# Kernel optimization log

Measured on AMD Instinct MI355X. Metric: run time of the kernel, lower is better.

The kernel has to match this reference:

```python
import jax, jax.numpy as jnp
import numpy as np

N_NODES = 16384


def gcn_conv(x, edge_index, W, b):
    """GCNConv: out = D^{-1/2} (A + I) D^{-1/2} (x @ W) + b."""
    n = x.shape[0]
    xw = x @ W  # [n, out_dim] -- transform before propagate (PyG order)
    loops = jnp.arange(n)
    src = jnp.concatenate([edge_index[0], loops])
    dst = jnp.concatenate([edge_index[1], loops])
    ones = jnp.ones(src.shape[0], dtype=xw.dtype)
    deg = jax.ops.segment_sum(ones, dst, num_segments=n)  # degree incl. self-loops
    dinv = jnp.where(deg > 0, jax.lax.rsqrt(deg), 0.0)
    norm = dinv[src] * dinv[dst]  # [E + n]
    msg = xw[src] * norm[:, None]  # gather + scale
    out = jax.ops.segment_sum(msg, dst, num_segments=n)  # scatter-add aggregate
    return out + b


def setup_inputs() -> dict:
    key = jax.random.key(0)
    ks = jax.random.split(key, 8)
    N, E, C = N_NODES, 524288, 7
    x = jax.random.normal(ks[0], (N, N), dtype=jnp.float32)
    edge_index = jax.random.randint(ks[1], (2, E), 0, N, dtype=jnp.int64)
    W1 = jax.random.normal(ks[2], (N, 50), dtype=jnp.float32) * (1.0 / np.sqrt(N))
    b1 = jnp.zeros((50,), dtype=jnp.float32)
    W2 = jax.random.normal(ks[3], (50, 2), dtype=jnp.float32) * (1.0 / np.sqrt(50))
    b2 = jnp.zeros((2,), dtype=jnp.float32)
    Wc = jax.random.normal(ks[4], (2, C), dtype=jnp.float32) * (1.0 / np.sqrt(2))
    bc = jnp.zeros((C,), dtype=jnp.float32)
    return {"x": x, "edge_index": edge_index, "W1": W1, "b1": b1,
            "W2": W2, "b2": b2, "Wc": Wc, "bc": bc}


def reference(x, edge_index, W1, b1, W2, b2, Wc, bc):
    h = jnp.tanh(gcn_conv(x, edge_index, W1, b1))   # [N, 50]
    h = jnp.tanh(gcn_conv(h, edge_index, W2, b2))   # [N, 2]
    out = h @ Wc + bc                               # [N, num_classes]
    return (out, h)
```

## Files before the change

kernel.cpp:

```cpp
#include <hip/hip_runtime.h>

typedef float  f32x4  __attribute__((ext_vector_type(4)));
typedef __bf16 bf16x8 __attribute__((ext_vector_type(8)));

#define N_NODES 16384
#define K_DIM   16384
#define H1_DIM  50
#define H1_PAD  64
#define CAP     160
#define OUT_OFF (N_NODES * 7)

typedef const __attribute__((address_space(1))) unsigned int* gas_ptr;
typedef __attribute__((address_space(3))) unsigned int* las_ptr;
__device__ __forceinline__ void gload_lds16(const void* g, void* l) {
  __builtin_amdgcn_global_load_lds((gas_ptr)g, (las_ptr)l, 16, 0, 0);
}

__global__ __launch_bounds__(256) void k_pre(const float* __restrict__ W1, __bf16* __restrict__ WT,
                                             const int* __restrict__ src, const int* __restrict__ dst,
                                             int E, int* cnt, int* bucket) {
  int t = threadIdx.x;
  if (blockIdx.x < 256) {
    __shared__ __bf16 lds[64][80];
    int k0 = blockIdx.x * 64;
    int rq = t >> 6, c = t & 63;
    for (int r = 0; r < 16; ++r) {
      int row = rq * 16 + r;
      __bf16 v = (__bf16)0.f;
      if (c < H1_DIM) v = (__bf16)W1[(size_t)(k0 + row) * H1_DIM + c];
      lds[c][row] = v;
    }
    __syncthreads();
    int cw = t >> 2, kq = (t & 3) * 16;
    __bf16* dp = WT + (size_t)cw * K_DIM + k0 + kq;
    *(bf16x8*)dp       = *(const bf16x8*)&lds[cw][kq];
    *((bf16x8*)dp + 1) = *(const bf16x8*)&lds[cw][kq + 8];
  } else {
    int e = (blockIdx.x - 256) * 256 + t;
    if (e < E) {
      int d = dst[e];
      int pos = atomicAdd(&cnt[d], 1);
      if (pos < CAP) bucket[(size_t)d * CAP + pos] = src[e];
    }
  }
}

__global__ __launch_bounds__(256) void k_gemm1(const float* __restrict__ x,
                                               const __bf16* __restrict__ WT,
                                               const int* __restrict__ cnt,
                                               float* __restrict__ xw) {
  __shared__ float  As[64 * 64];
  __shared__ __bf16 Bs[64 * 64];
  int tid = threadIdx.x;
  int w = tid >> 6, l = tid & 63;
  int l15 = l & 15, l7 = l & 7, g2 = l >> 4;
  int row0 = blockIdx.x * 64;
  int kbase = blockIdx.y * 4096;

  int a_row = w * 4 + (l >> 4);
  int b_col = w * 8 + (l >> 3);
  int m_row = w * 16 + l15;

  int phase = ((blockIdx.x + (blockIdx.x >> 3) + blockIdx.y) & 3) << 4;

  f32x4 acc0 = {0,0,0,0}, acc1 = {0,0,0,0}, acc2 = {0,0,0,0}, acc3 = {0,0,0,0};

  for (int it = 0; it < 64; ++it) {
    int ks = (it + phase) & 63;
    int kk = kbase + ks * 64;
#pragma unroll
    for (int c = 0; c < 4; ++c) {
      int r = c * 16 + a_row;
      const float* gp = x + (size_t)(row0 + r) * K_DIM + kk + ((l15 ^ (r & 15)) << 2);
      gload_lds16(gp, &As[c * 1024 + w * 256]);
    }
#pragma unroll
    for (int c = 0; c < 2; ++c) {
      int col = c * 32 + b_col;
      const __bf16* gp = WT + (size_t)col * K_DIM + kk + ((l7 ^ (col & 7)) << 3);
      gload_lds16(gp, &Bs[c * 2048 + w * 512]);
    }
    __syncthreads();
#pragma unroll
    for (int s = 0; s < 2; ++s) {
      int c0 = s * 8 + g2 * 2;
      f32x4 a0 = *(const f32x4*)&As[m_row * 64 + (((c0    ) ^ l15) << 2)];
      f32x4 a1 = *(const f32x4*)&As[m_row * 64 + (((c0 + 1) ^ l15) << 2)];
      bf16x8 af;
      af[0] = (__bf16)a0[0]; af[1] = (__bf16)a0[1]; af[2] = (__bf16)a0[2]; af[3] = (__bf16)a0[3];
      af[4] = (__bf16)a1[0]; af[5] = (__bf16)a1[1]; af[6] = (__bf16)a1[2]; af[7] = (__bf16)a1[3];
      int cb = (s * 4 + g2) ^ l7;
      bf16x8 b0 = *(const bf16x8*)&Bs[(     l15) * 64 + (cb << 3)];
      bf16x8 b1 = *(const bf16x8*)&Bs[(16 + l15) * 64 + (cb << 3)];
      bf16x8 b2 = *(const bf16x8*)&Bs[(32 + l15) * 64 + (cb << 3)];
      bf16x8 b3 = *(const bf16x8*)&Bs[(48 + l15) * 64 + (cb << 3)];
      acc0 = __builtin_amdgcn_mfma_f32_16x16x32_bf16(af, b0, acc0, 0, 0, 0);
      acc1 = __builtin_amdgcn_mfma_f32_16x16x32_bf16(af, b1, acc1, 0, 0, 0);
      acc2 = __builtin_amdgcn_mfma_f32_16x16x32_bf16(af, b2, acc2, 0, 0, 0);
      acc3 = __builtin_amdgcn_mfma_f32_16x16x32_bf16(af, b3, acc3, 0, 0, 0);
    }
    __syncthreads();
  }

  int crow = row0 + w * 16 + g2 * 4;
#pragma unroll
  for (int j = 0; j < 4; ++j) {
    float dv = rsqrtf((float)(cnt[crow + j] + 1));
    size_t rb = (size_t)(crow + j) * H1_PAD + l15;
    atomicAdd(&xw[rb],      acc0[j] * dv);
    atomicAdd(&xw[rb + 16], acc1[j] * dv);
    atomicAdd(&xw[rb + 32], acc2[j] * dv);
    atomicAdd(&xw[rb + 48], acc3[j] * dv);
  }
}

__global__ __launch_bounds__(256) void k_agg1(const float* __restrict__ xw,
                                              const int* __restrict__ cnt,
                                              const int* __restrict__ bucket,
                                              const float* __restrict__ b1,
                                              const float* __restrict__ W2,
                                              float* __restrict__ xw2s) {
  int tid = threadIdx.x;
  int nid = blockIdx.x * 4 + (tid >> 6);
  int j = tid & 63;
  float acc = xw[(size_t)nid * H1_PAD + j];
  int cn0 = cnt[nid];
  int cn = cn0 > CAP ? CAP : cn0;
  const int* bp = bucket + (size_t)nid * CAP;
  int p = 0;
  for (; p + 3 < cn; p += 4) {
    int s0 = bp[p], s1 = bp[p + 1], s2 = bp[p + 2], s3 = bp[p + 3];
    acc += xw[(size_t)s0 * H1_PAD + j];
    acc += xw[(size_t)s1 * H1_PAD + j];
    acc += xw[(size_t)s2 * H1_PAD + j];
    acc += xw[(size_t)s3 * H1_PAD + j];
  }
  for (; p < cn; ++p) acc += xw[(size_t)bp[p] * H1_PAD + j];

  float dv = rsqrtf((float)(cn0 + 1));
  float bj = (j < H1_DIM) ? b1[j] : 0.f;
  float h = tanhf(dv * acc + bj);
  float w0 = (j < H1_DIM) ? W2[j * 2]     : 0.f;
  float w1 = (j < H1_DIM) ? W2[j * 2 + 1] : 0.f;
  float a0 = h * w0, a1 = h * w1;
#pragma unroll
  for (int off = 32; off >= 1; off >>= 1) {
    a0 += __shfl_xor(a0, off);
    a1 += __shfl_xor(a1, off);
  }
  if (j == 0) {
    xw2s[nid * 2]     = a0 * dv;
    xw2s[nid * 2 + 1] = a1 * dv;
  }
}

__global__ __launch_bounds__(256) void k_final(const float* __restrict__ xw2s,
                                               const int* __restrict__ cnt,
                                               const int* __restrict__ bucket,
                                               const float* __restrict__ b2,
                                               const float* __restrict__ Wc,
                                               const float* __restrict__ bc,
                                               float* __restrict__ dout) {
  int tid = threadIdx.x;
  int g = tid >> 4, r = tid & 15;
  int nid = blockIdx.x * 16 + g;
  int cn0 = cnt[nid];
  int cn = cn0 > CAP ? CAP : cn0;
  const int* bp = bucket + (size_t)nid * CAP;
  float a0 = 0.f, a1 = 0.f;
  for (int p = r; p < cn; p += 16) {
    int sc = bp[p];
    a0 += xw2s[sc * 2];
    a1 += xw2s[sc * 2 + 1];
  }
#pragma unroll
  for (int off = 8; off >= 1; off >>= 1) {
    a0 += __shfl_xor(a0, off, 16);
    a1 += __shfl_xor(a1, off, 16);
  }
  if (r == 0) {
    a0 += xw2s[nid * 2];
    a1 += xw2s[nid * 2 + 1];
    float dv = rsqrtf((float)(cn0 + 1));
    float h0  = tanhf(dv * a0 + b2[0]);
    float h1v = tanhf(dv * a1 + b2[1]);
#pragma unroll
    for (int j = 0; j < 7; ++j)
      dout[nid * 7 + j] = h0 * Wc[j] + h1v * Wc[7 + j] + bc[j];
    dout[OUT_OFF + nid * 2]     = h0;
    dout[OUT_OFF + nid * 2 + 1] = h1v;
  }
}

extern "C" void kernel_launch(void* const* d_in, const int* in_sizes, int n_in,
                              void* d_out, int out_size, void* d_ws, size_t ws_size,
                              hipStream_t stream) {
  const float* x  = (const float*)d_in[0];
  const int*   ei = (const int*)d_in[1];
  const float* W1 = (const float*)d_in[2];
  const float* b1 = (const float*)d_in[3];
  const float* W2 = (const float*)d_in[4];
  const float* b2 = (const float*)d_in[5];
  const float* Wc = (const float*)d_in[6];
  const float* bc = (const float*)d_in[7];
  float* dout = (float*)d_out;
  const int E = in_sizes[1] / 2;
  const int* esrc = ei;
  const int* edst = ei + E;

  char* ws = (char*)d_ws;
  float*  xw      = (float*)(ws + 0x0000000);
  __bf16* WT      = (__bf16*)(ws + 0x0400000);
  int*    cnt     = (int*)(ws + 0x0600000);
  int*    bucket  = (int*)(ws + 0x0620000);
  float*  xw2s    = (float*)(ws + 0x1100000);

  hipMemsetAsync(cnt, 0, N_NODES * sizeof(int), stream);
  hipMemsetAsync(xw, 0, N_NODES * H1_PAD * sizeof(float), stream);
  k_pre<<<256 + (E + 255) / 256, 256, 0, stream>>>(W1, WT, esrc, edst, E, cnt, bucket);
  k_gemm1<<<dim3(256, 4), 256, 0, stream>>>(x, WT, cnt, xw);
  k_agg1<<<N_NODES / 4, 256, 0, stream>>>(xw, cnt, bucket, b1, W2, xw2s);
  k_final<<<N_NODES / 16, 256, 0, stream>>>(xw2s, cnt, bucket, b2, Wc, bc, dout);
}
```

Measured before the change: 272.2 us.

## Give each wave private LDS tiles and drop block-wide barriers in GEMM1

Each of the four waves in the GEMM1 block now loads its own 16-row A slice and a private full copy of the 64-column B tile into LDS. It waits only on its own loads with s_waitcnt instead of two __syncthreads per k-step, and the phase-rotated k order is removed. The aim is to take block-level barrier stalls off the loop so waves can run independently. In exchange, B tile traffic to LDS rises fourfold and LDS use grows. Without a barrier after compute, a wave's next-iteration async loads could overwrite LDS its own pending reads still need, since ordering relies only on the in-wave waitcnt.

```diff
diff --git a/kernel.cpp b/kernel.cpp
--- a/kernel.cpp
+++ b/kernel.cpp
@@ -49,57 +49,56 @@
                                                const __bf16* __restrict__ WT,
                                                const int* __restrict__ cnt,
                                                float* __restrict__ xw) {
-  __shared__ float  As[64 * 64];
-  __shared__ __bf16 Bs[64 * 64];
+  __shared__ float  As[4][16 * 64];
+  __shared__ __bf16 Bs[4][64 * 64];
   int tid = threadIdx.x;
   int w = tid >> 6, l = tid & 63;
   int l15 = l & 15, l7 = l & 7, g2 = l >> 4;
   int row0 = blockIdx.x * 64;
   int kbase = blockIdx.y * 4096;
 
-  int a_row = w * 4 + (l >> 4);
-  int b_col = w * 8 + (l >> 3);
-  int m_row = w * 16 + l15;
-
-  int phase = ((blockIdx.x + (blockIdx.x >> 3) + blockIdx.y) & 3) << 4;
+  int a_rl = l >> 4;
+  int b_cl = l >> 3;
+
+  const float* ga[4];
+#pragma unroll
+  for (int c = 0; c < 4; ++c) {
+    int rl = (c << 2) | a_rl;
+    ga[c] = x + (size_t)(row0 + w * 16 + rl) * K_DIM + kbase + ((l15 ^ rl) << 2);
+  }
+  const __bf16* gb = WT + (size_t)b_cl * K_DIM + kbase + ((l7 ^ b_cl) << 3);
+
+  float*  asw = &As[w][0];
+  __bf16* bsw = &Bs[w][0];
 
   f32x4 acc0 = {0,0,0,0}, acc1 = {0,0,0,0}, acc2 = {0,0,0,0}, acc3 = {0,0,0,0};
 
-  for (int it = 0; it < 64; ++it) {
-    int ks = (it + phase) & 63;
-    int kk = kbase + ks * 64;
-#pragma unroll
-    for (int c = 0; c < 4; ++c) {
-      int r = c * 16 + a_row;
-      const float* gp = x + (size_t)(row0 + r) * K_DIM + kk + ((l15 ^ (r & 15)) << 2);
-      gload_lds16(gp, &As[c * 1024 + w * 256]);
-    }
-#pragma unroll
-    for (int c = 0; c < 2; ++c) {
-      int col = c * 32 + b_col;
-      const __bf16* gp = WT + (size_t)col * K_DIM + kk + ((l7 ^ (col & 7)) << 3);
-      gload_lds16(gp, &Bs[c * 2048 + w * 512]);
-    }
-    __syncthreads();
+  for (int ks = 0; ks < 64; ++ks) {
+    int kk = ks * 64;
+#pragma unroll
+    for (int c = 0; c < 4; ++c) gload_lds16(ga[c] + kk, asw + c * 256);
+#pragma unroll
+    for (int c = 0; c < 8; ++c) gload_lds16(gb + (size_t)c * 8 * K_DIM + kk, bsw + c * 512);
+    asm volatile("s_waitcnt vmcnt(0)" ::: "memory");
+    __builtin_amdgcn_sched_barrier(0);
 #pragma unroll
     for (int s = 0; s < 2; ++s) {
       int c0 = s * 8 + g2 * 2;
-      f32x4 a0 = *(const f32x4*)&As[m_row * 64 + (((c0    ) ^ l15) << 2)];
-      f32x4 a1 = *(const f32x4*)&As[m_row * 64 + (((c0 + 1) ^ l15) << 2)];
+      f32x4 a0 = *(const f32x4*)&asw[l15 * 64 + (((c0    ) ^ l15) << 2)];
+      f32x4 a1 = *(const f32x4*)&asw[l15 * 64 + (((c0 + 1) ^ l15) << 2)];
       bf16x8 af;
       af[0] = (__bf16)a0[0]; af[1] = (__bf16)a0[1]; af[2] = (__bf16)a0[2]; af[3] = (__bf16)a0[3];
       af[4] = (__bf16)a1[0]; af[5] = (__bf16)a1[1]; af[6] = (__bf16)a1[2]; af[7] = (__bf16)a1[3];
       int cb = (s * 4 + g2) ^ l7;
-      bf16x8 b0 = *(const bf16x8*)&Bs[(     l15) * 64 + (cb << 3)];
-      bf16x8 b1 = *(const bf16x8*)&Bs[(16 + l15) * 64 + (cb << 3)];
-      bf16x8 b2 = *(const bf16x8*)&Bs[(32 + l15) * 64 + (cb << 3)];
-      bf16x8 b3 = *(const bf16x8*)&Bs[(48 + l15) * 64 + (cb << 3)];
+      bf16x8 b0 = *(const bf16x8*)&bsw[(     l15) * 64 + (cb << 3)];
+      bf16x8 b1 = *(const bf16x8*)&bsw[(16 + l15) * 64 + (cb << 3)];
+      bf16x8 b2 = *(const bf16x8*)&bsw[(32 + l15) * 64 + (cb << 3)];
+      bf16x8 b3 = *(const bf16x8*)&bsw[(48 + l15) * 64 + (cb << 3)];
       acc0 = __builtin_amdgcn_mfma_f32_16x16x32_bf16(af, b0, acc0, 0, 0, 0);
       acc1 = __builtin_amdgcn_mfma_f32_16x16x32_bf16(af, b1, acc1, 0, 0, 0);
       acc2 = __builtin_amdgcn_mfma_f32_16x16x32_bf16(af, b2, acc2, 0, 0, 0);
       acc3 = __builtin_amdgcn_mfma_f32_16x16x32_bf16(af, b3, acc3, 0, 0, 0);
     }
-    __syncthreads();
   }
 
   int crow = row0 + w * 16 + g2 * 4;
```

Result: slower. 330.8 us (+21.5%).

## Fold memsets into init kernel and overlap edge bucketing with GEMM

Applied to the files above, without the earlier changes.

The two hipMemsetAsync calls are replaced by extra blocks in a new init kernel that also transposes W1. Edge bucketing moves out of the preprocessing kernel and into the GEMM launch as extra blocks, so it runs alongside the GEMM tiles. Because the degree counts are now still being built while the GEMM runs, the source-side D^-1/2 scale moves out of the GEMM epilogue and into the aggregation loop. That adds one cnt load and one rsqrt per gathered neighbor. The aim is fewer launches and hiding the bucketing time, at the cost of extra gather work in k_agg1.

```diff
diff --git a/kernel.cpp b/kernel.cpp
--- a/kernel.cpp
+++ b/kernel.cpp
@@ -16,13 +16,12 @@
   __builtin_amdgcn_global_load_lds((gas_ptr)g, (las_ptr)l, 16, 0, 0);
 }
 
-__global__ __launch_bounds__(256) void k_pre(const float* __restrict__ W1, __bf16* __restrict__ WT,
-                                             const int* __restrict__ src, const int* __restrict__ dst,
-                                             int E, int* cnt, int* bucket) {
-  int t = threadIdx.x;
-  if (blockIdx.x < 256) {
+__global__ __launch_bounds__(256) void k_init(const float* __restrict__ W1, __bf16* __restrict__ WT,
+                                              float* __restrict__ xw, int* __restrict__ cnt) {
+  int t = threadIdx.x, b = blockIdx.x;
+  if (b < 256) {
     __shared__ __bf16 lds[64][80];
-    int k0 = blockIdx.x * 64;
+    int k0 = b * 64;
     int rq = t >> 6, c = t & 63;
     for (int r = 0; r < 16; ++r) {
       int row = rq * 16 + r;
@@ -35,33 +34,44 @@
     __bf16* dp = WT + (size_t)cw * K_DIM + k0 + kq;
     *(bf16x8*)dp       = *(const bf16x8*)&lds[cw][kq];
     *((bf16x8*)dp + 1) = *(const bf16x8*)&lds[cw][kq + 8];
+  } else if (b < 1280) {
+    int i = (b - 256) * 1024 + t * 4;
+    *(f32x4*)&xw[i] = (f32x4){0.f, 0.f, 0.f, 0.f};
   } else {
-    int e = (blockIdx.x - 256) * 256 + t;
+    cnt[(b - 1280) * 256 + t] = 0;
+  }
+}
+
+__global__ __launch_bounds__(256) void k_gemm1(const float* __restrict__ x,
+                                               const __bf16* __restrict__ WT,
+                                               const int* __restrict__ src,
+                                               const int* __restrict__ dst, int E,
+                                               int* cnt, int* bucket,
+                                               float* __restrict__ xw) {
+  __shared__ float  As[64 * 64];
+  __shared__ __bf16 Bs[64 * 64];
+  int tid = threadIdx.x;
+  int gid = blockIdx.x;
+  if (gid >= 1024) {
+    int e = (gid - 1024) * 256 + tid;
     if (e < E) {
       int d = dst[e];
       int pos = atomicAdd(&cnt[d], 1);
       if (pos < CAP) bucket[(size_t)d * CAP + pos] = src[e];
     }
-  }
-}
-
-__global__ __launch_bounds__(256) void k_gemm1(const float* __restrict__ x,
-                                               const __bf16* __restrict__ WT,
-                                               const int* __restrict__ cnt,
-                                               float* __restrict__ xw) {
-  __shared__ float  As[64 * 64];
-  __shared__ __bf16 Bs[64 * 64];
-  int tid = threadIdx.x;
+    return;
+  }
+  int bx = gid >> 2, by = gid & 3;
   int w = tid >> 6, l = tid & 63;
   int l15 = l & 15, l7 = l & 7, g2 = l >> 4;
-  int row0 = blockIdx.x * 64;
-  int kbase = blockIdx.y * 4096;
+  int row0 = bx * 64;
+  int kbase = by * 4096;
 
   int a_row = w * 4 + (l >> 4);
   int b_col = w * 8 + (l >> 3);
   int m_row = w * 16 + l15;
 
-  int phase = ((blockIdx.x + (blockIdx.x >> 3) + blockIdx.y) & 3) << 4;
+  int phase = ((bx + (bx >> 3) + by) & 3) << 4;
 
   f32x4 acc0 = {0,0,0,0}, acc1 = {0,0,0,0}, acc2 = {0,0,0,0}, acc3 = {0,0,0,0};
 
@@ -105,12 +115,11 @@
   int crow = row0 + w * 16 + g2 * 4;
 #pragma unroll
   for (int j = 0; j < 4; ++j) {
-    float dv = rsqrtf((float)(cnt[crow + j] + 1));
     size_t rb = (size_t)(crow + j) * H1_PAD + l15;
-    atomicAdd(&xw[rb],      acc0[j] * dv);
-    atomicAdd(&xw[rb + 16], acc1[j] * dv);
-    atomicAdd(&xw[rb + 32], acc2[j] * dv);
-    atomicAdd(&xw[rb + 48], acc3[j] * dv);
+    atomicAdd(&xw[rb],      acc0[j]);
+    atomicAdd(&xw[rb + 16], acc1[j]);
+    atomicAdd(&xw[rb + 32], acc2[j]);
+    atomicAdd(&xw[rb + 48], acc3[j]);
   }
 }
 
@@ -123,21 +132,28 @@
   int tid = threadIdx.x;
   int nid = blockIdx.x * 4 + (tid >> 6);
   int j = tid & 63;
-  float acc = xw[(size_t)nid * H1_PAD + j];
   int cn0 = cnt[nid];
   int cn = cn0 > CAP ? CAP : cn0;
+  float dv = rsqrtf((float)(cn0 + 1));
+  float acc = dv * xw[(size_t)nid * H1_PAD + j];
   const int* bp = bucket + (size_t)nid * CAP;
   int p = 0;
   for (; p + 3 < cn; p += 4) {
     int s0 = bp[p], s1 = bp[p + 1], s2 = bp[p + 2], s3 = bp[p + 3];
-    acc += xw[(size_t)s0 * H1_PAD + j];
-    acc += xw[(size_t)s1 * H1_PAD + j];
-    acc += xw[(size_t)s2 * H1_PAD + j];
-    acc += xw[(size_t)s3 * H1_PAD + j];
-  }
-  for (; p < cn; ++p) acc += xw[(size_t)bp[p] * H1_PAD + j];
-
-  float dv = rsqrtf((float)(cn0 + 1));
+    float d0 = rsqrtf((float)(cnt[s0] + 1));
+    float d1 = rsqrtf((float)(cnt[s1] + 1));
+    float d2 = rsqrtf((float)(cnt[s2] + 1));
+    float d3 = rsqrtf((float)(cnt[s3] + 1));
+    acc += d0 * xw[(size_t)s0 * H1_PAD + j];
+    acc += d1 * xw[(size_t)s1 * H1_PAD + j];
+    acc += d2 * xw[(size_t)s2 * H1_PAD + j];
+    acc += d3 * xw[(size_t)s3 * H1_PAD + j];
+  }
+  for (; p < cn; ++p) {
+    int sc = bp[p];
+    acc += rsqrtf((float)(cnt[sc] + 1)) * xw[(size_t)sc * H1_PAD + j];
+  }
+
   float bj = (j < H1_DIM) ? b1[j] : 0.f;
   float h = tanhf(dv * acc + bj);
   float w0 = (j < H1_DIM) ? W2[j * 2]     : 0.f;
@@ -215,10 +231,8 @@
   int*    bucket  = (int*)(ws + 0x0620000);
   float*  xw2s    = (float*)(ws + 0x1100000);
 
-  hipMemsetAsync(cnt, 0, N_NODES * sizeof(int), stream);
-  hipMemsetAsync(xw, 0, N_NODES * H1_PAD * sizeof(float), stream);
-  k_pre<<<256 + (E + 255) / 256, 256, 0, stream>>>(W1, WT, esrc, edst, E, cnt, bucket);
-  k_gemm1<<<dim3(256, 4), 256, 0, stream>>>(x, WT, cnt, xw);
+  k_init<<<1344, 256, 0, stream>>>(W1, WT, xw, cnt);
+  k_gemm1<<<1024 + (E + 255) / 256, 256, 0, stream>>>(x, WT, esrc, edst, E, cnt, bucket, xw);
   k_agg1<<<N_NODES / 4, 256, 0, stream>>>(xw, cnt, bucket, b1, W2, xw2s);
   k_final<<<N_NODES / 16, 256, 0, stream>>>(xw2s, cnt, bucket, b2, Wc, bc, dout);
 }
```

After: 294.9 us. +8.3%, slower.
